# Kernel optimization log

Hardware: AMD Instinct MI355X
Metric: run time of the kernel (lower is better)

The kernel has to match this reference:

```python
import jax, jax.numpy as jnp
import numpy as np

N = 50000
E = 800000
IN_FEAT = 128
HIDDEN = 64
HEADS = 4
CLASSES = 40
NEG_SLOPE = 0.2


def setup_inputs() -> dict:
    key = jax.random.key(0)
    ks = jax.random.split(key, 12)
    x = jax.random.normal(ks[0], (N, IN_FEAT), dtype=jnp.float32)
    # edge_index without self loops (module removes then re-adds them)
    src = jax.random.randint(ks[1], (E,), 0, N)
    off = jax.random.randint(ks[2], (E,), 1, N)
    dst = (src + off) % N  # guaranteed dst != src
    edge_index = jnp.stack([src, dst]).astype(jnp.int64)
    g = 1.0 / np.sqrt(IN_FEAT)
    lin1_w = jax.random.normal(ks[3], (IN_FEAT, HEADS * HIDDEN), dtype=jnp.float32) * g
    lin1_b = jax.random.normal(ks[4], (HEADS * HIDDEN,), dtype=jnp.float32) * 0.01
    att1 = jax.random.normal(ks[5], (1, HEADS, 2 * HIDDEN), dtype=jnp.float32) * (1.0 / np.sqrt(2 * HIDDEN))
    bias1 = jnp.zeros((HEADS * HIDDEN,), dtype=jnp.float32)
    lin2_w = jax.random.normal(ks[6], (HEADS * HIDDEN, CLASSES), dtype=jnp.float32) * (1.0 / np.sqrt(HEADS * HIDDEN))
    lin2_b = jax.random.normal(ks[7], (CLASSES,), dtype=jnp.float32) * 0.01
    att2 = jax.random.normal(ks[8], (1, 1, 2 * CLASSES), dtype=jnp.float32) * (1.0 / np.sqrt(2 * CLASSES))
    bias2 = jnp.zeros((CLASSES,), dtype=jnp.float32)
    return {"x": x, "edge_index": edge_index, "lin1_w": lin1_w, "lin1_b": lin1_b,
            "att1": att1, "bias1": bias1, "lin2_w": lin2_w, "lin2_b": lin2_b,
            "att2": att2, "bias2": bias2}


def gat_conv(x, src, dst, W, b_lin, att, bias, heads, oc):
    n = x.shape[0]
    fea = (x @ W + b_lin).reshape(n, heads, oc)            # [N, H, C]
    # attention logits: (cat([x_i, x_j]) * att).sum(-1) decomposed per node
    score_i = jnp.einsum('nhc,hc->nh', fea, att[0, :, :oc])  # target half
    score_j = jnp.einsum('nhc,hc->nh', fea, att[0, :, oc:])  # source half
    alpha = score_i[dst] + score_j[src]                    # [E, H]
    alpha = jax.nn.leaky_relu(alpha, NEG_SLOPE)
    # segment softmax over target node
    amax = jax.ops.segment_max(alpha, dst, num_segments=n)
    alpha = jnp.exp(alpha - amax[dst])
    asum = jax.ops.segment_sum(alpha, dst, num_segments=n)
    alpha = alpha / (asum[dst] + 1e-16)
    # message = x_j * alpha; scatter-add to target
    msg = fea[src] * alpha[:, :, None]                     # [E, H, C]
    out = jax.ops.segment_sum(msg, dst, num_segments=n)
    return out.reshape(n, heads * oc) + bias               # concat=True


def reference(x, edge_index, lin1_w, lin1_b, att1, bias1, lin2_w, lin2_b, att2, bias2):
    n = x.shape[0]
    loop = jnp.arange(n, dtype=edge_index.dtype)
    src = jnp.concatenate([edge_index[0], loop])  # add self loops
    dst = jnp.concatenate([edge_index[1], loop])
    h = gat_conv(x, src, dst, lin1_w, lin1_b, att1, bias1, HEADS, HIDDEN)
    h = jax.nn.relu(h)
    h = gat_conv(h, src, dst, lin2_w, lin2_b, att2, bias2, 1, CLASSES)
    return jax.nn.softmax(h, axis=1)
```

## Files before the change

### kernel.cpp

```cpp
#include <hip/hip_runtime.h>
#include <hip/hip_fp16.h>

#define NN 50000
#define NE 800000
#define INFEAT 128
#define F1 256
#define HID 64
#define CLS 40
#define NEGS 0.2f
#define NB 49
#define GBM 128
#define GB1 1564
#define HB  1563

__device__ __forceinline__ float lrelu(float x) { return x > 0.0f ? x : NEGS * x; }

struct alignas(8) H4 { __half2 a, b; };
struct alignas(16) H8 { __half2 a, b, c, d; };

typedef __attribute__((ext_vector_type(8))) _Float16 f16x8;
typedef __attribute__((ext_vector_type(4))) float f32x4;

__global__ __launch_bounds__(256) void gemm1_hist_k(const float* __restrict__ A,
                                                    const float* __restrict__ W,
                                                    const float* __restrict__ b,
                                                    const float* __restrict__ att1,
                                                    __half* __restrict__ feah,
                                                    float* __restrict__ sI,
                                                    float* __restrict__ sJ,
                                                    const int* __restrict__ dst,
                                                    int* __restrict__ deg,
                                                    int* __restrict__ ord) {
    __shared__ __align__(16) _Float16 As[128][40];
    __shared__ __align__(16) _Float16 Ws[64][40];
    int bx = blockIdx.x;
    int tid = threadIdx.x;
    if (bx >= GB1) {
        int base = (bx - GB1) * 512;
        int e0 = base + tid, e1 = base + 256 + tid;
        if (e0 < NE) ord[e0] = atomicAdd(&deg[dst[e0]], 1);
        if (e1 < NE) ord[e1] = atomicAdd(&deg[dst[e1]], 1);
        return;
    }
    int wid = tid >> 6, lane = tid & 63;
    int row0 = (bx >> 2) * GBM;
    int head = bx & 3;
    int colB = head * 64;
    int lr = lane & 15;
    int lg = lane >> 4;

    f32x4 acc[2][4];
    #pragma unroll
    for (int rt = 0; rt < 2; ++rt)
        #pragma unroll
        for (int ct = 0; ct < 4; ++ct) acc[rt][ct] = (f32x4){0.f, 0.f, 0.f, 0.f};

    int wcol = tid & 63;
    int wkg  = tid >> 6;

    for (int k0 = 0; k0 < INFEAT; k0 += 32) {
        #pragma unroll
        for (int i = 0; i < 4; ++i) {
            int q = tid + 256 * i;
            int r = q >> 3;
            int c4 = (q & 7) * 4;
            int grow = row0 + r;
            float4 v = make_float4(0.f, 0.f, 0.f, 0.f);
            if (grow < NN) v = *(const float4*)&A[(size_t)grow * INFEAT + k0 + c4];
            As[r][c4 + 0] = (_Float16)v.x; As[r][c4 + 1] = (_Float16)v.y;
            As[r][c4 + 2] = (_Float16)v.z; As[r][c4 + 3] = (_Float16)v.w;
        }
        {
            f16x8 wv;
            #pragma unroll
            for (int j = 0; j < 8; ++j)
                wv[j] = (_Float16)W[(size_t)(k0 + wkg * 8 + j) * F1 + colB + wcol];
            *(f16x8*)&Ws[wcol][wkg * 8] = wv;
        }
        __syncthreads();
        f16x8 afrag[2], bfrag[4];
        #pragma unroll
        for (int rt = 0; rt < 2; ++rt)
            afrag[rt] = *(const f16x8*)&As[wid * 32 + rt * 16 + lr][lg * 8];
        #pragma unroll
        for (int ct = 0; ct < 4; ++ct)
            bfrag[ct] = *(const f16x8*)&Ws[ct * 16 + lr][lg * 8];
        #pragma unroll
        for (int rt = 0; rt < 2; ++rt)
            #pragma unroll
            for (int ct = 0; ct < 4; ++ct)
                acc[rt][ct] = __builtin_amdgcn_mfma_f32_16x16x32_f16(
                    afrag[rt], bfrag[ct], acc[rt][ct], 0, 0, 0);
        __syncthreads();
    }
    float aIv[4], aJv[4], bv[4];
    #pragma unroll
    for (int ct = 0; ct < 4; ++ct) {
        int cin = ct * 16 + lr;
        aIv[ct] = att1[head * 2 * HID + cin];
        aJv[ct] = att1[head * 2 * HID + HID + cin];
        bv[ct]  = b[colB + cin];
    }
    #pragma unroll
    for (int rt = 0; rt < 2; ++rt) {
        #pragma unroll
        for (int i = 0; i < 4; ++i) {
            int grow = row0 + wid * 32 + rt * 16 + lg * 4 + i;
            float o[4];
            float sIp = 0.f, sJp = 0.f;
            #pragma unroll
            for (int ct = 0; ct < 4; ++ct) {
                o[ct] = acc[rt][ct][i] + bv[ct];
                sIp += o[ct] * aIv[ct];
                sJp += o[ct] * aJv[ct];
            }
            #pragma unroll
            for (int off = 1; off < 16; off <<= 1) {
                sIp += __shfl_xor(sIp, off);
                sJp += __shfl_xor(sJp, off);
            }
            if (grow < NN) {
                #pragma unroll
                for (int ct = 0; ct < 4; ++ct)
                    feah[(size_t)grow * F1 + colB + ct * 16 + lr] = __float2half(o[ct]);
                if (lr == 0) {
                    sI[grow * 4 + head] = sIp;
                    sJ[grow * 4 + head] = sJp;
                }
            }
        }
    }
}

__global__ __launch_bounds__(1024) void scan1_k(const int* __restrict__ deg,
                                                int* __restrict__ row_off,
                                                int* __restrict__ bsum) {
    __shared__ int tmp[1024];
    int tid = threadIdx.x;
    int gid = blockIdx.x * 1024 + tid;
    int v = (gid < NN) ? deg[gid] : 0;
    tmp[tid] = v;
    __syncthreads();
    #pragma unroll
    for (int off = 1; off < 1024; off <<= 1) {
        int t = (tid >= off) ? tmp[tid - off] : 0;
        __syncthreads();
        tmp[tid] += t;
        __syncthreads();
    }
    if (gid <= NN) row_off[gid] = tmp[tid] - v;
    if (tid == 1023) bsum[blockIdx.x] = tmp[1023];
}

__global__ void scan2_k(const int* __restrict__ bsum, int* __restrict__ bpref) {
    int tid = threadIdx.x;
    int orig = (tid < NB) ? bsum[tid] : 0;
    int v = orig;
    #pragma unroll
    for (int off = 1; off < 64; off <<= 1) {
        int t = __shfl_up(v, off);
        if (tid >= off) v += t;
    }
    if (tid < NB) bpref[tid] = v - orig;
}

#define SC_T (NE / 2)
__global__ void scatter_k(const int* __restrict__ src, const int* __restrict__ dst,
                          const int* __restrict__ ord, const int* __restrict__ row_off,
                          const int* __restrict__ bpref,
                          const float* __restrict__ sI, const float* __restrict__ sJ,
                          int* __restrict__ csr, float4* __restrict__ ep4) {
    int t = blockIdx.x * blockDim.x + threadIdx.x;
    if (t >= SC_T) return;
    int e0 = t, e1 = t + SC_T;
    int s0 = src[e0], s1 = src[e1];
    int d0 = dst[e0], d1 = dst[e1];
    int p0 = row_off[d0] + bpref[d0 >> 10] + ord[e0];
    int p1 = row_off[d1] + bpref[d1 >> 10] + ord[e1];
    float4 si0 = *(const float4*)&sI[d0 * 4];
    float4 si1 = *(const float4*)&sI[d1 * 4];
    float4 sj0 = *(const float4*)&sJ[s0 * 4];
    float4 sj1 = *(const float4*)&sJ[s1 * 4];
    float4 r0, r1;
    r0.x = __expf(lrelu(si0.x + sj0.x)); r0.y = __expf(lrelu(si0.y + sj0.y));
    r0.z = __expf(lrelu(si0.z + sj0.z)); r0.w = __expf(lrelu(si0.w + sj0.w));
    r1.x = __expf(lrelu(si1.x + sj1.x)); r1.y = __expf(lrelu(si1.y + sj1.y));
    r1.z = __expf(lrelu(si1.z + sj1.z)); r1.w = __expf(lrelu(si1.w + sj1.w));
    csr[p0] = s0; csr[p1] = s1;
    ep4[p0] = r0; ep4[p1] = r1;
}

__global__ __launch_bounds__(256, 6) void agg1_k(const __half* __restrict__ feah,
                                                 const float* __restrict__ sI,
                                                 const float* __restrict__ sJ,
                                                 const float* __restrict__ epf,
                                                 const int* __restrict__ row_off,
                                                 const int* __restrict__ bpref,
                                                 const int* __restrict__ csr,
                                                 const float* __restrict__ bias,
                                                 __half* __restrict__ out) {
    int wid = threadIdx.x >> 6, lane = threadIdx.x & 63;
    int n = blockIdx.x * 4 + wid;
    if (n >= NN) return;
    int h = lane >> 4;
    int c = lane * 4;
    float p = __expf(lrelu(sI[n * 4 + h] + sJ[n * 4 + h]));
    float asum = p;
    H4 vs = *(const H4*)&feah[(size_t)n * F1 + c];
    float2 sx = __half22float2(vs.a), sy = __half22float2(vs.b);
    float4 acc = make_float4(sx.x * p, sx.y * p, sy.x * p, sy.y * p);
    int beg = row_off[n] + bpref[n >> 10];
    int end = row_off[n + 1] + bpref[(n + 1) >> 10];
    int e = beg;
    for (; e + 8 <= end; e += 8) {
        int s0 = csr[e + 0], s1 = csr[e + 1], s2 = csr[e + 2], s3 = csr[e + 3];
        int s4 = csr[e + 4], s5 = csr[e + 5], s6 = csr[e + 6], s7 = csr[e + 7];
        float p0 = epf[(e + 0) * 4 + h], p1 = epf[(e + 1) * 4 + h];
        float p2 = epf[(e + 2) * 4 + h], p3 = epf[(e + 3) * 4 + h];
        float p4 = epf[(e + 4) * 4 + h], p5 = epf[(e + 5) * 4 + h];
        float p6 = epf[(e + 6) * 4 + h], p7 = epf[(e + 7) * 4 + h];
        H4 v0 = *(const H4*)&feah[(size_t)s0 * F1 + c];
        H4 v1 = *(const H4*)&feah[(size_t)s1 * F1 + c];
        H4 v2 = *(const H4*)&feah[(size_t)s2 * F1 + c];
        H4 v3 = *(const H4*)&feah[(size_t)s3 * F1 + c];
        H4 v4 = *(const H4*)&feah[(size_t)s4 * F1 + c];
        H4 v5 = *(const H4*)&feah[(size_t)s5 * F1 + c];
        H4 v6 = *(const H4*)&feah[(size_t)s6 * F1 + c];
        H4 v7 = *(const H4*)&feah[(size_t)s7 * F1 + c];
        asum += ((p0 + p1) + (p2 + p3)) + ((p4 + p5) + (p6 + p7));
        float2 x0 = __half22float2(v0.a), y0 = __half22float2(v0.b);
        float2 x1 = __half22float2(v1.a), y1 = __half22float2(v1.b);
        float2 x2 = __half22float2(v2.a), y2 = __half22float2(v2.b);
        float2 x3 = __half22float2(v3.a), y3 = __half22float2(v3.b);
        float2 x4 = __half22float2(v4.a), y4 = __half22float2(v4.b);
        float2 x5 = __half22float2(v5.a), y5 = __half22float2(v5.b);
        float2 x6 = __half22float2(v6.a), y6 = __half22float2(v6.b);
        float2 x7 = __half22float2(v7.a), y7 = __half22float2(v7.b);
        acc.x += (x0.x * p0 + x1.x * p1 + x2.x * p2 + x3.x * p3)
               + (x4.x * p4 + x5.x * p5 + x6.x * p6 + x7.x * p7);
        acc.y += (x0.y * p0 + x1.y * p1 + x2.y * p2 + x3.y * p3)
               + (x4.y * p4 + x5.y * p5 + x6.y * p6 + x7.y * p7);
        acc.z += (y0.x * p0 + y1.x * p1 + y2.x * p2 + y3.x * p3)
               + (y4.x * p4 + y5.x * p5 + y6.x * p6 + y7.x * p7);
        acc.w += (y0.y * p0 + y1.y * p1 + y2.y * p2 + y3.y * p3)
               + (y4.y * p4 + y5.y * p5 + y6.y * p6 + y7.y * p7);
    }
    for (; e + 4 <= end; e += 4) {
        int s0 = csr[e], s1 = csr[e + 1], s2 = csr[e + 2], s3 = csr[e + 3];
        float p0 = epf[(e + 0) * 4 + h], p1 = epf[(e + 1) * 4 + h];
        float p2 = epf[(e + 2) * 4 + h], p3 = epf[(e + 3) * 4 + h];
        H4 v0 = *(const H4*)&feah[(size_t)s0 * F1 + c];
        H4 v1 = *(const H4*)&feah[(size_t)s1 * F1 + c];
        H4 v2 = *(const H4*)&feah[(size_t)s2 * F1 + c];
        H4 v3 = *(const H4*)&feah[(size_t)s3 * F1 + c];
        asum += (p0 + p1) + (p2 + p3);
        float2 x0 = __half22float2(v0.a), y0 = __half22float2(v0.b);
        float2 x1 = __half22float2(v1.a), y1 = __half22float2(v1.b);
        float2 x2 = __half22float2(v2.a), y2 = __half22float2(v2.b);
        float2 x3 = __half22float2(v3.a), y3 = __half22float2(v3.b);
        acc.x += x0.x * p0 + x1.x * p1 + x2.x * p2 + x3.x * p3;
        acc.y += x0.y * p0 + x1.y * p1 + x2.y * p2 + x3.y * p3;
        acc.z += y0.x * p0 + y1.x * p1 + y2.x * p2 + y3.x * p3;
        acc.w += y0.y * p0 + y1.y * p1 + y2.y * p2 + y3.y * p3;
    }
    for (; e < end; ++e) {
        int s = csr[e];
        float pe = epf[e * 4 + h];
        asum += pe;
        H4 v = *(const H4*)&feah[(size_t)s * F1 + c];
        float2 x = __half22float2(v.a), y = __half22float2(v.b);
        acc.x += x.x * pe; acc.y += x.y * pe;
        acc.z += y.x * pe; acc.w += y.y * pe;
    }
    float inv = 1.0f / (asum + 1e-16f);
    float4 bv = *(const float4*)&bias[c];
    H4 o4;
    o4.a = __floats2half2_rn(fmaxf(acc.x * inv + bv.x, 0.f),
                             fmaxf(acc.y * inv + bv.y, 0.f));
    o4.b = __floats2half2_rn(fmaxf(acc.z * inv + bv.z, 0.f),
                             fmaxf(acc.w * inv + bv.w, 0.f));
    *(H4*)&out[(size_t)n * F1 + c] = o4;
}

#define G2M 128
__global__ __launch_bounds__(256) void gemm2_k(const __half* __restrict__ h1h,
                                               const float* __restrict__ W2,
                                               const float* __restrict__ b2,
                                               const float* __restrict__ att2,
                                               __half* __restrict__ fea2h,
                                               float* __restrict__ s2I,
                                               float* __restrict__ s2J) {
    __shared__ __align__(16) _Float16 Ws2[48][264];
    __shared__ __align__(16) _Float16 As2[128][40];
    int tid = threadIdx.x;
    int wid = tid >> 6, lane = tid & 63;
    int lr = lane & 15, lg = lane >> 4;
    int row0 = blockIdx.x * G2M;
    for (int q = tid; q < 48 * 32; q += 256) {
        int col = q >> 5;
        int kg  = q & 31;
        f16x8 wv;
        #pragma unroll
        for (int j = 0; j < 8; ++j) {
            int k = kg * 8 + j;
            wv[j] = (col < CLS) ? (_Float16)W2[(size_t)k * CLS + col] : (_Float16)0.f;
        }
        *(f16x8*)&Ws2[col][kg * 8] = wv;
    }
    f32x4 acc[2][3];
    #pragma unroll
    for (int rt = 0; rt < 2; ++rt)
        #pragma unroll
        for (int ct = 0; ct < 3; ++ct) acc[rt][ct] = (f32x4){0.f, 0.f, 0.f, 0.f};

    for (int k0 = 0; k0 < F1; k0 += 32) {
        #pragma unroll
        for (int i = 0; i < 2; ++i) {
            int q = tid + 256 * i;
            int r = q >> 2;
            int c8 = (q & 3) * 8;
            int grow = row0 + r;
            f16x8 v;
            if (grow < NN) v = *(const f16x8*)&h1h[(size_t)grow * F1 + k0 + c8];
            else {
                #pragma unroll
                for (int j = 0; j < 8; ++j) v[j] = (_Float16)0.f;
            }
            *(f16x8*)&As2[r][c8] = v;
        }
        __syncthreads();
        f16x8 af[2], bf[3];
        #pragma unroll
        for (int rt = 0; rt < 2; ++rt)
            af[rt] = *(const f16x8*)&As2[wid * 32 + rt * 16 + lr][lg * 8];
        #pragma unroll
        for (int ct = 0; ct < 3; ++ct)
            bf[ct] = *(const f16x8*)&Ws2[ct * 16 + lr][k0 + lg * 8];
        #pragma unroll
        for (int rt = 0; rt < 2; ++rt)
            #pragma unroll
            for (int ct = 0; ct < 3; ++ct)
                acc[rt][ct] = __builtin_amdgcn_mfma_f32_16x16x32_f16(
                    af[rt], bf[ct], acc[rt][ct], 0, 0, 0);
        __syncthreads();
    }
    float bcol[3], aIc[3], aJc[3];
    bool valid[3];
    #pragma unroll
    for (int ct = 0; ct < 3; ++ct) {
        int col = ct * 16 + lr;
        valid[ct] = col < CLS;
        int cc = valid[ct] ? col : 0;
        bcol[ct] = b2[cc];
        aIc[ct] = valid[ct] ? att2[cc] : 0.f;
        aJc[ct] = valid[ct] ? att2[CLS + cc] : 0.f;
    }
    #pragma unroll
    for (int rt = 0; rt < 2; ++rt) {
        #pragma unroll
        for (int i = 0; i < 4; ++i) {
            int grow = row0 + wid * 32 + rt * 16 + lg * 4 + i;
            float o[3];
            float sIp = 0.f, sJp = 0.f;
            #pragma unroll
            for (int ct = 0; ct < 3; ++ct) {
                o[ct] = acc[rt][ct][i] + bcol[ct];
                sIp += o[ct] * aIc[ct];
                sJp += o[ct] * aJc[ct];
            }
            #pragma unroll
            for (int off = 1; off < 16; off <<= 1) {
                sIp += __shfl_xor(sIp, off);
                sJp += __shfl_xor(sJp, off);
            }
            if (grow < NN) {
                #pragma unroll
                for (int ct = 0; ct < 3; ++ct)
                    if (valid[ct])
                        fea2h[(size_t)grow * CLS + ct * 16 + lr] = __float2half(o[ct]);
                if (lr == 0) {
                    s2I[grow] = sIp;
                    s2J[grow] = sJp;
                }
            }
        }
    }
}

__global__ __launch_bounds__(256) void agg2_k(const __half* __restrict__ fea2h,
                                              const float* __restrict__ s2I,
                                              const float* __restrict__ s2J,
                                              const int* __restrict__ row_off,
                                              const int* __restrict__ bpref,
                                              const int* __restrict__ csr,
                                              const float* __restrict__ bias2,
                                              float* __restrict__ out) {
    int wid = threadIdx.x >> 6, lane = threadIdx.x & 63;
    int n = blockIdx.x * 4 + wid;
    if (n >= NN) return;
    float si = s2I[n], sjn = s2J[n];
    int c = lane < CLS ? lane : 0;
    float p = __expf(lrelu(si + sjn));
    float asum = p;
    float acc = __half2float(fea2h[(size_t)n * CLS + c]) * p;
    int beg = row_off[n] + bpref[n >> 10];
    int end = row_off[n + 1] + bpref[(n + 1) >> 10];
    int e = beg;
    for (; e + 8 <= end; e += 8) {
        int s0 = csr[e + 0], s1 = csr[e + 1], s2 = csr[e + 2], s3 = csr[e + 3];
        int s4 = csr[e + 4], s5 = csr[e + 5], s6 = csr[e + 6], s7 = csr[e + 7];
        float a0 = s2J[s0], a1 = s2J[s1], a2 = s2J[s2], a3 = s2J[s3];
        float a4 = s2J[s4], a5 = s2J[s5], a6 = s2J[s6], a7 = s2J[s7];
        __half f0 = fea2h[(size_t)s0 * CLS + c];
        __half f1 = fea2h[(size_t)s1 * CLS + c];
        __half f2 = fea2h[(size_t)s2 * CLS + c];
        __half f3 = fea2h[(size_t)s3 * CLS + c];
        __half f4 = fea2h[(size_t)s4 * CLS + c];
        __half f5 = fea2h[(size_t)s5 * CLS + c];
        __half f6 = fea2h[(size_t)s6 * CLS + c];
        __half f7 = fea2h[(size_t)s7 * CLS + c];
        float p0 = __expf(lrelu(si + a0));
        float p1 = __expf(lrelu(si + a1));
        float p2 = __expf(lrelu(si + a2));
        float p3 = __expf(lrelu(si + a3));
        float p4 = __expf(lrelu(si + a4));
        float p5 = __expf(lrelu(si + a5));
        float p6 = __expf(lrelu(si + a6));
        float p7 = __expf(lrelu(si + a7));
        asum += ((p0 + p1) + (p2 + p3)) + ((p4 + p5) + (p6 + p7));
        acc += (__half2float(f0) * p0 + __half2float(f1) * p1
              + __half2float(f2) * p2 + __half2float(f3) * p3)
             + (__half2float(f4) * p4 + __half2float(f5) * p5
              + __half2float(f6) * p6 + __half2float(f7) * p7);
    }
    for (; e + 4 <= end; e += 4) {
        int s0 = csr[e], s1 = csr[e + 1], s2 = csr[e + 2], s3 = csr[e + 3];
        float p0 = __expf(lrelu(si + s2J[s0]));
        float p1 = __expf(lrelu(si + s2J[s1]));
        float p2 = __expf(lrelu(si + s2J[s2]));
        float p3 = __expf(lrelu(si + s2J[s3]));
        __half f0 = fea2h[(size_t)s0 * CLS + c];
        __half f1 = fea2h[(size_t)s1 * CLS + c];
        __half f2 = fea2h[(size_t)s2 * CLS + c];
        __half f3 = fea2h[(size_t)s3 * CLS + c];
        asum += (p0 + p1) + (p2 + p3);
        acc += __half2float(f0) * p0 + __half2float(f1) * p1
             + __half2float(f2) * p2 + __half2float(f3) * p3;
    }
    for (; e < end; ++e) {
        int s = csr[e];
        float pe = __expf(lrelu(si + s2J[s]));
        asum += pe;
        acc += __half2float(fea2h[(size_t)s * CLS + c]) * pe;
    }
    float row = acc / (asum + 1e-16f) + bias2[c];
    float v = (lane < CLS) ? row : -3.0e38f;
    float vm = v;
    #pragma unroll
    for (int off = 32; off; off >>= 1) vm = fmaxf(vm, __shfl_xor(vm, off));
    float ex = (lane < CLS) ? __expf(v - vm) : 0.f;
    float es = ex;
    #pragma unroll
    for (int off = 32; off; off >>= 1) es += __shfl_xor(es, off);
    if (lane < CLS) out[(size_t)n * CLS + lane] = ex / es;
}

extern "C" void kernel_launch(void* const* d_in, const int* in_sizes, int n_in,
                              void* d_out, int out_size, void* d_ws, size_t ws_size,
                              hipStream_t stream) {
    const float* x     = (const float*)d_in[0];
    const int*   ei    = (const int*)d_in[1];
    const float* w1    = (const float*)d_in[2];
    const float* b1    = (const float*)d_in[3];
    const float* att1  = (const float*)d_in[4];
    const float* bias1 = (const float*)d_in[5];
    const float* w2    = (const float*)d_in[6];
    const float* b2    = (const float*)d_in[7];
    const float* att2  = (const float*)d_in[8];
    const float* bias2 = (const float*)d_in[9];
    const int* src = ei;
    const int* dst = ei + NE;
    float* out = (float*)d_out;

    char* p = (char*)d_ws;
    auto alloc = [&](size_t bytes) {
        char* r = p;
        p += (bytes + 255) & ~(size_t)255;
        return r;
    };
    __half* fea1h = (__half*)alloc((size_t)NN * F1 * 2);
    __half* h1h   = (__half*)alloc((size_t)NN * F1 * 2);
    float* sI1    = (float*)alloc((size_t)NN * 4 * 4);
    float* sJ1    = (float*)alloc((size_t)NN * 4 * 4);
    __half* fea2h = (__half*)alloc((size_t)NN * CLS * 2);
    float* s2I    = (float*)alloc((size_t)NN * 4);
    float* s2J    = (float*)alloc((size_t)NN * 4);
    int*   deg    = (int*)alloc((size_t)NN * 4);
    int*   row_off= (int*)alloc((size_t)(NN + 1) * 4);
    int*   bsum   = (int*)alloc((size_t)NB * 4);
    int*   bpref  = (int*)alloc((size_t)NB * 4);
    int*   ord    = (int*)alloc((size_t)NE * 4);
    int*   csr    = (int*)alloc((size_t)NE * 4);
    float* ep1    = (float*)alloc((size_t)NE * 4 * 4);

    hipMemsetAsync(deg, 0, (size_t)NN * 4, stream);

    gemm1_hist_k<<<GB1 + HB, 256, 0, stream>>>(x, w1, b1, att1, fea1h, sI1, sJ1,
                                               dst, deg, ord);
    scan1_k<<<NB, 1024, 0, stream>>>(deg, row_off, bsum);
    scan2_k<<<1, 64, 0, stream>>>(bsum, bpref);
    scatter_k<<<(SC_T + 255) / 256, 256, 0, stream>>>(src, dst, ord, row_off, bpref,
                                                      sI1, sJ1, csr, (float4*)ep1);
    agg1_k<<<(NN + 3) / 4, 256, 0, stream>>>(fea1h, sI1, sJ1, ep1, row_off, bpref,
                                             csr, bias1, h1h);
    gemm2_k<<<(NN + G2M - 1) / G2M, 256, 0, stream>>>(h1h, w2, b2, att2, fea2h, s2I, s2J);
    agg2_k<<<(NN + 3) / 4, 256, 0, stream>>>(fea2h, s2I, s2J, row_off, bpref,
                                             csr, bias2, out);
}
```

Baseline: 217.4 us.

## Preload full W slice into LDS, vectorize A staging, front-load histogram blocks

The GEMM1 blocks now load the whole 128x64 weight slice for their head into shared memory once, instead of reloading a 32-row piece on every k-step. The A tile is staged with two float4 loads per thread and one 16-byte half8 LDS store, replacing scalar half stores. Histogram blocks now come first in the grid and each handles 1024 edges, so there are fewer of them and the atomic work is dispatched early. The cost is more LDS per block (about 30 KB), which may lower occupancy, plus a larger up-front weight load before the first MFMA.

```diff
diff --git a/kernel.cpp b/kernel.cpp
--- a/kernel.cpp
+++ b/kernel.cpp
@@ -11,7 +11,7 @@
 #define NB 49
 #define GBM 128
 #define GB1 1564
-#define HB  1563
+#define HB4 782
 
 __device__ __forceinline__ float lrelu(float x) { return x > 0.0f ? x : NEGS * x; }
 
@@ -32,50 +32,64 @@
                                                     int* __restrict__ deg,
                                                     int* __restrict__ ord) {
     __shared__ __align__(16) _Float16 As[128][40];
-    __shared__ __align__(16) _Float16 Ws[64][40];
+    __shared__ __align__(16) _Float16 Ws[4][64][40];
     int bx = blockIdx.x;
     int tid = threadIdx.x;
-    if (bx >= GB1) {
-        int base = (bx - GB1) * 512;
-        int e0 = base + tid, e1 = base + 256 + tid;
+    if (bx < HB4) {
+        int base = bx * 1024 + tid;
+        int e0 = base, e1 = base + 256, e2 = base + 512, e3 = base + 768;
         if (e0 < NE) ord[e0] = atomicAdd(&deg[dst[e0]], 1);
         if (e1 < NE) ord[e1] = atomicAdd(&deg[dst[e1]], 1);
+        if (e2 < NE) ord[e2] = atomicAdd(&deg[dst[e2]], 1);
+        if (e3 < NE) ord[e3] = atomicAdd(&deg[dst[e3]], 1);
         return;
     }
+    int gb = bx - HB4;
     int wid = tid >> 6, lane = tid & 63;
-    int row0 = (bx >> 2) * GBM;
-    int head = bx & 3;
+    int row0 = (gb >> 2) * GBM;
+    int head = gb & 3;
     int colB = head * 64;
     int lr = lane & 15;
     int lg = lane >> 4;
 
+    for (int q = tid; q < 1024; q += 256) {
+        int col = q & 63;
+        int kg  = (q >> 6) & 3;
+        int ks  = q >> 8;
+        f16x8 wv;
+        #pragma unroll
+        for (int j = 0; j < 8; ++j)
+            wv[j] = (_Float16)W[(size_t)(ks * 32 + kg * 8 + j) * F1 + colB + col];
+        *(f16x8*)&Ws[ks][col][kg * 8] = wv;
+    }
+
     f32x4 acc[2][4];
     #pragma unroll
     for (int rt = 0; rt < 2; ++rt)
         #pragma unroll
         for (int ct = 0; ct < 4; ++ct) acc[rt][ct] = (f32x4){0.f, 0.f, 0.f, 0.f};
 
-    int wcol = tid & 63;
-    int wkg  = tid >> 6;
-
-    for (int k0 = 0; k0 < INFEAT; k0 += 32) {
-        #pragma unroll
-        for (int i = 0; i < 4; ++i) {
+    for (int ks = 0; ks < 4; ++ks) {
+        int k0 = ks * 32;
+        #pragma unroll
+        for (int i = 0; i < 2; ++i) {
             int q = tid + 256 * i;
-            int r = q >> 3;
-            int c4 = (q & 7) * 4;
+            int r = q >> 2;
+            int c8 = (q & 3) * 8;
             int grow = row0 + r;
-            float4 v = make_float4(0.f, 0.f, 0.f, 0.f);
-            if (grow < NN) v = *(const float4*)&A[(size_t)grow * INFEAT + k0 + c4];
-            As[r][c4 + 0] = (_Float16)v.x; As[r][c4 + 1] = (_Float16)v.y;
-            As[r][c4 + 2] = (_Float16)v.z; As[r][c4 + 3] = (_Float16)v.w;
-        }
-        {
-            f16x8 wv;
-            #pragma unroll
-            for (int j = 0; j < 8; ++j)
-                wv[j] = (_Float16)W[(size_t)(k0 + wkg * 8 + j) * F1 + colB + wcol];
-            *(f16x8*)&Ws[wcol][wkg * 8] = wv;
+            f16x8 hv;
+            if (grow < NN) {
+                float4 v0 = *(const float4*)&A[(size_t)grow * INFEAT + k0 + c8];
+                float4 v1 = *(const float4*)&A[(size_t)grow * INFEAT + k0 + c8 + 4];
+                hv[0] = (_Float16)v0.x; hv[1] = (_Float16)v0.y;
+                hv[2] = (_Float16)v0.z; hv[3] = (_Float16)v0.w;
+                hv[4] = (_Float16)v1.x; hv[5] = (_Float16)v1.y;
+                hv[6] = (_Float16)v1.z; hv[7] = (_Float16)v1.w;
+            } else {
+                #pragma unroll
+                for (int j = 0; j < 8; ++j) hv[j] = (_Float16)0.f;
+            }
+            *(f16x8*)&As[r][c8] = hv;
         }
         __syncthreads();
         f16x8 afrag[2], bfrag[4];
@@ -84,7 +98,7 @@
             afrag[rt] = *(const f16x8*)&As[wid * 32 + rt * 16 + lr][lg * 8];
         #pragma unroll
         for (int ct = 0; ct < 4; ++ct)
-            bfrag[ct] = *(const f16x8*)&Ws[ct * 16 + lr][lg * 8];
+            bfrag[ct] = *(const f16x8*)&Ws[ks][ct * 16 + lr][lg * 8];
         #pragma unroll
         for (int rt = 0; rt < 2; ++rt)
             #pragma unroll
@@ -505,8 +519,8 @@
 
     hipMemsetAsync(deg, 0, (size_t)NN * 4, stream);
 
-    gemm1_hist_k<<<GB1 + HB, 256, 0, stream>>>(x, w1, b1, att1, fea1h, sI1, sJ1,
-                                               dst, deg, ord);
+    gemm1_hist_k<<<HB4 + GB1, 256, 0, stream>>>(x, w1, b1, att1, fea1h, sI1, sJ1,
+                                                dst, deg, ord);
     scan1_k<<<NB, 1024, 0, stream>>>(deg, row_off, bsum);
     scan2_k<<<1, 64, 0, stream>>>(bsum, bpref);
     scatter_k<<<(SC_T + 255) / 256, 256, 0, stream>>>(src, dst, ord, row_off, bpref,
```

After: 217.9 us. About the same (+0.2%).
